# Performance work log

Hardware: AMD Instinct MI355X
Metric: run time of the kernel (lower is better)

## Reference

```python
import jax, jax.numpy as jnp
import numpy as np

HEAD_DIM = 256
NUM_HEADS = 16
NUM_KV_HEADS = 8
EPS = 1e-6
SCALING = 256 ** -0.5  # query_pre_attn_scalar
SOFTCAP = 50.0
NEG_INF = -2.3819763e38


def setup_inputs() -> dict:
    key = jax.random.key(0)
    ks = jax.random.split(key, 8)
    B, S, HID, MAXS = 1, 2048, 3072, 4096
    hidden_states = jax.random.normal(ks[0], (B, S, HID), dtype=jnp.float32)
    # RoPE tables (complex freqs_cis represented as cos/sin), base 10000
    inv_freq = 1.0 / (10000.0 ** (np.arange(0, HEAD_DIM, 2, dtype=np.float32) / HEAD_DIM))
    t = np.arange(S, dtype=np.float32)
    ang = np.outer(t, inv_freq)  # [S, D/2]
    freqs_cos = jnp.asarray(np.cos(ang), dtype=jnp.float32)
    freqs_sin = jnp.asarray(np.sin(ang), dtype=jnp.float32)
    kv_write_indices = jnp.arange(S, dtype=jnp.int32)
    k_cache = jnp.zeros((B, MAXS, NUM_KV_HEADS, HEAD_DIM), dtype=jnp.float32)
    v_cache = jnp.zeros((B, MAXS, NUM_KV_HEADS, HEAD_DIM), dtype=jnp.float32)
    # causal mask over cache slots: query i may attend cache slot j iff j <= i
    i = jnp.arange(S)[:, None]
    j = jnp.arange(MAXS)[None, :]
    mask = jnp.where(j <= i, 0.0, NEG_INF).astype(jnp.float32)[None, None]  # [1,1,S,MAXS]
    sd = 1.0 / np.sqrt(HID)
    wq = jax.random.normal(ks[1], (HID, NUM_HEADS * HEAD_DIM), dtype=jnp.float32) * sd
    wk = jax.random.normal(ks[2], (HID, NUM_KV_HEADS * HEAD_DIM), dtype=jnp.float32) * sd
    wv = jax.random.normal(ks[3], (HID, NUM_KV_HEADS * HEAD_DIM), dtype=jnp.float32) * sd
    wo = jax.random.normal(ks[4], (NUM_HEADS * HEAD_DIM, HID), dtype=jnp.float32) * (1.0 / np.sqrt(NUM_HEADS * HEAD_DIM))
    q_norm_w = jax.random.normal(ks[5], (HEAD_DIM,), dtype=jnp.float32) * 0.02
    k_norm_w = jax.random.normal(ks[6], (HEAD_DIM,), dtype=jnp.float32) * 0.02
    return dict(hidden_states=hidden_states, freqs_cos=freqs_cos, freqs_sin=freqs_sin,
                kv_write_indices=kv_write_indices, k_cache=k_cache, v_cache=v_cache,
                mask=mask, wq=wq, wk=wk, wv=wv, wo=wo, q_norm_w=q_norm_w, k_norm_w=k_norm_w)


def _rmsnorm(x, w):
    xf = x.astype(jnp.float32)
    n = xf * jax.lax.rsqrt(jnp.mean(xf * xf, axis=-1, keepdims=True) + EPS)
    return (n * (1.0 + w.astype(jnp.float32))).astype(x.dtype)


def _rope(x, cos, sin):
    # x: [B,S,H,D]; complex rotation on (first half, second half) pairs
    D2 = x.shape[-1] // 2
    xr, xi = x[..., :D2], x[..., D2:]
    cos = cos[None, :, None, :]
    sin = sin[None, :, None, :]
    return jnp.concatenate([xr * cos - xi * sin, xr * sin + xi * cos], axis=-1).astype(x.dtype)


def reference(hidden_states, freqs_cos, freqs_sin, kv_write_indices, k_cache, v_cache,
              mask, wq, wk, wv, wo, q_norm_w, k_norm_w):
    B, S, _ = hidden_states.shape
    xq = (hidden_states @ wq).reshape(B, S, NUM_HEADS, HEAD_DIM)
    xk = (hidden_states @ wk).reshape(B, S, NUM_KV_HEADS, HEAD_DIM)
    xv = (hidden_states @ wv).reshape(B, S, NUM_KV_HEADS, HEAD_DIM)
    xq = _rmsnorm(xq, q_norm_w)
    xk = _rmsnorm(xk, k_norm_w)
    xq = _rope(xq, freqs_cos, freqs_sin)
    xk = _rope(xk, freqs_cos, freqs_sin)
    # KV-cache write (index_copy_ on dim 1)
    k_cache = k_cache.at[:, kv_write_indices].set(xk)
    v_cache = v_cache.at[:, kv_write_indices].set(xv)
    rep = NUM_HEADS // NUM_KV_HEADS
    key = jnp.repeat(k_cache, rep, axis=2)    # [B,MAXS,H,D]
    value = jnp.repeat(v_cache, rep, axis=2)
    scores = jnp.einsum('bqhd,bkhd->bhqk', xq * SCALING, key)
    scores = jnp.tanh(scores / SOFTCAP) * SOFTCAP
    scores = scores + mask
    probs = jax.nn.softmax(scores.astype(jnp.float32), axis=-1).astype(xq.dtype)
    out = jnp.einsum('bhqk,bkhd->bqhd', probs, value).reshape(B, S, NUM_HEADS * HEAD_DIM)
    return out @ wo
```

## Files before the change

### kernel.cpp

```cpp
#include <hip/hip_runtime.h>
#include <hip/hip_bf16.h>

#define S_LEN 2048
#define HID   3072
#define NH    16
#define NKV   8
#define HD    256
#define EPSV  1e-6f
#define SCALING 0.0625f
#define SOFTCAP 50.0f

typedef __attribute__((ext_vector_type(8))) short bf16x8;
typedef __attribute__((ext_vector_type(4))) float f32x4;

__device__ __forceinline__ unsigned short f2bf(float f) {
  union { float f; unsigned u; } x; x.f = f;
  unsigned r = x.u + 0x7FFFu + ((x.u >> 16) & 1u);
  return (unsigned short)(r >> 16);
}

__device__ __forceinline__ void gload_lds16(const void* g, void* l) {
  __builtin_amdgcn_global_load_lds((const __attribute__((address_space(1))) void*)g,
                                   (__attribute__((address_space(3))) void*)l, 16, 0, 0);
}

__global__ __launch_bounds__(256) void conv_b(const float* __restrict__ in,
                                              unsigned short* __restrict__ out, int n) {
  int i = (blockIdx.x * 256 + threadIdx.x) * 4;
  if (i >= n) return;
  float4 v = *(const float4*)(in + i);
  ushort4 o;
  o.x = f2bf(v.x); o.y = f2bf(v.y); o.z = f2bf(v.z); o.w = f2bf(v.w);
  *(ushort4*)(out + i) = o;
}

__global__ __launch_bounds__(256) void conv_t(const float* __restrict__ W,
                                              unsigned short* __restrict__ WT,
                                              int K, int N) {
  __shared__ float tile[32][33];
  int tx = threadIdx.x & 31, ty = threadIdx.x >> 5;
  int n0 = blockIdx.x * 32, k0 = blockIdx.y * 32;
#pragma unroll
  for (int j = 0; j < 4; j++)
    tile[ty + j * 8][tx] = W[(size_t)(k0 + ty + j * 8) * N + n0 + tx];
  __syncthreads();
#pragma unroll
  for (int j = 0; j < 4; j++)
    WT[(size_t)(n0 + ty + j * 8) * K + k0 + tx] = f2bf(tile[tx][ty + j * 8]);
}

__global__ __launch_bounds__(256) void tr_bf16(const unsigned short* __restrict__ in,
                                               unsigned short* __restrict__ out,
                                               int R, int C) {
  __shared__ unsigned short tile[32][33];
  int tx = threadIdx.x & 31, ty = threadIdx.x >> 5;
  int c0 = blockIdx.x * 32, r0 = blockIdx.y * 32;
#pragma unroll
  for (int j = 0; j < 4; j++)
    tile[ty + j * 8][tx] = in[(size_t)(r0 + ty + j * 8) * C + c0 + tx];
  __syncthreads();
#pragma unroll
  for (int j = 0; j < 4; j++)
    out[(size_t)(c0 + ty + j * 8) * R + r0 + tx] = tile[tx][ty + j * 8];
}

__global__ __launch_bounds__(256) void gemm_qkv(const unsigned short* __restrict__ A,
                                                const unsigned short* __restrict__ B,
                                                float* __restrict__ XQ,
                                                float* __restrict__ XK,
                                                unsigned short* __restrict__ Vb) {
  const int K = HID;
  __shared__ unsigned short As[128 * 32];
  __shared__ unsigned short Bs[128 * 32];
  const int t = threadIdx.x;
  const int w = t >> 6, l = t & 63;
  const int m0 = blockIdx.y * 128, n0 = blockIdx.x * 128;
  const int wr = (w >> 1) * 64, wc = (w & 1) * 64;
  const int lr = l & 15, lk = (l >> 4) * 8;
  f32x4 acc[4][4] = {};

  const int e0 = t * 8;
  const int ar0 = e0 >> 5, ac0 = e0 & 31;
  const size_t abase = (size_t)(m0 + ar0) * K + ac0;
  const size_t bbase = (size_t)(n0 + ar0) * K + ac0;

  for (int k0 = 0; k0 < K; k0 += 32) {
    gload_lds16(A + abase + k0, As + e0);
    gload_lds16(A + abase + (size_t)64 * K + k0, As + e0 + 2048);
    gload_lds16(B + bbase + k0, Bs + e0);
    gload_lds16(B + bbase + (size_t)64 * K + k0, Bs + e0 + 2048);
    __syncthreads();
    bf16x8 af[4], bfv[4];
#pragma unroll
    for (int i = 0; i < 4; i++)
      af[i] = *(const bf16x8*)(As + (wr + i * 16 + lr) * 32 + lk);
#pragma unroll
    for (int i = 0; i < 4; i++)
      bfv[i] = *(const bf16x8*)(Bs + (wc + i * 16 + lr) * 32 + lk);
#pragma unroll
    for (int i = 0; i < 4; i++)
#pragma unroll
      for (int j = 0; j < 4; j++)
        acc[i][j] = __builtin_amdgcn_mfma_f32_16x16x32_bf16(af[i], bfv[j], acc[i][j], 0, 0, 0);
    __syncthreads();
  }

  const int rq = (l >> 4) * 4;
#pragma unroll
  for (int i = 0; i < 4; i++)
#pragma unroll
    for (int j = 0; j < 4; j++) {
      int mrow = m0 + wr + i * 16 + rq;
      int ncol = n0 + wc + j * 16 + lr;
      if (ncol < 4096) {
#pragma unroll
        for (int r = 0; r < 4; r++)
          XQ[(size_t)(mrow + r) * 4096 + ncol] = acc[i][j][r];
      } else if (ncol < 6144) {
#pragma unroll
        for (int r = 0; r < 4; r++)
          XK[(size_t)(mrow + r) * 2048 + ncol - 4096] = acc[i][j][r];
      } else {
#pragma unroll
        for (int r = 0; r < 4; r++)
          Vb[(size_t)(mrow + r) * 2048 + ncol - 6144] = f2bf(acc[i][j][r]);
      }
    }
}

__global__ __launch_bounds__(256) void gemm_nt(const unsigned short* __restrict__ A,
                                               const unsigned short* __restrict__ B,
                                               float* __restrict__ Cf,
                                               int M, int N, int K) {
  __shared__ unsigned short As[128 * 32];
  __shared__ unsigned short Bs[128 * 32];
  const int t = threadIdx.x;
  const int w = t >> 6, l = t & 63;
  const int m0 = blockIdx.y * 128, n0 = blockIdx.x * 128;
  const int wr = (w >> 1) * 64, wc = (w & 1) * 64;
  const int lr = l & 15, lk = (l >> 4) * 8;
  f32x4 acc[4][4] = {};

  const int e0 = t * 8;
  const int ar0 = e0 >> 5, ac0 = e0 & 31;
  const size_t abase = (size_t)(m0 + ar0) * K + ac0;
  const size_t bbase = (size_t)(n0 + ar0) * K + ac0;

  for (int k0 = 0; k0 < K; k0 += 32) {
    gload_lds16(A + abase + k0, As + e0);
    gload_lds16(A + abase + (size_t)64 * K + k0, As + e0 + 2048);
    gload_lds16(B + bbase + k0, Bs + e0);
    gload_lds16(B + bbase + (size_t)64 * K + k0, Bs + e0 + 2048);
    __syncthreads();
    bf16x8 af[4], bfv[4];
#pragma unroll
    for (int i = 0; i < 4; i++)
      af[i] = *(const bf16x8*)(As + (wr + i * 16 + lr) * 32 + lk);
#pragma unroll
    for (int i = 0; i < 4; i++)
      bfv[i] = *(const bf16x8*)(Bs + (wc + i * 16 + lr) * 32 + lk);
#pragma unroll
    for (int i = 0; i < 4; i++)
#pragma unroll
      for (int j = 0; j < 4; j++)
        acc[i][j] = __builtin_amdgcn_mfma_f32_16x16x32_bf16(af[i], bfv[j], acc[i][j], 0, 0, 0);
    __syncthreads();
  }

  const int rq = (l >> 4) * 4;
#pragma unroll
  for (int i = 0; i < 4; i++)
#pragma unroll
    for (int j = 0; j < 4; j++) {
      int mrow = m0 + wr + i * 16 + rq;
      int ncol = n0 + wc + j * 16 + lr;
#pragma unroll
      for (int r = 0; r < 4; r++)
        Cf[(size_t)(mrow + r) * N + ncol] = acc[i][j][r];
    }
}

__global__ __launch_bounds__(256) void norm_rope(const float* __restrict__ x,
                                                 unsigned short* __restrict__ out,
                                                 const float* __restrict__ w,
                                                 const float* __restrict__ fc,
                                                 const float* __restrict__ fs,
                                                 int heads_per_tok, float scale) {
  __shared__ float sh[256];
  __shared__ float red[4];
  int row = blockIdx.x;
  int t = threadIdx.x;
  float v = x[(size_t)row * 256 + t];
  float ss = v * v;
#pragma unroll
  for (int off = 32; off > 0; off >>= 1) ss += __shfl_down(ss, off);
  if ((t & 63) == 0) red[t >> 6] = ss;
  __syncthreads();
  float tot = red[0] + red[1] + red[2] + red[3];
  float rn = rsqrtf(tot * (1.0f / 256.0f) + EPSV);
  sh[t] = v * rn * (1.0f + w[t]);
  __syncthreads();
  if (t < 128) {
    int s = row / heads_per_tok;
    int h = row - s * heads_per_tok;
    size_t ob = ((size_t)h * S_LEN + s) * HD;
    float xr = sh[t], xi = sh[t + 128];
    float c = fc[(size_t)s * 128 + t], sn = fs[(size_t)s * 128 + t];
    out[ob + t]       = f2bf((xr * c - xi * sn) * scale);
    out[ob + t + 128] = f2bf((xr * sn + xi * c) * scale);
  }
}

__global__ __launch_bounds__(256) void attn(const unsigned short* __restrict__ Q,
                                            const unsigned short* __restrict__ Kc,
                                            const unsigned short* __restrict__ VT,
                                            unsigned short* __restrict__ O) {
  __shared__ unsigned short Ks[2][32 * 256];
  __shared__ unsigned short Vs[2][256 * 32];
  __shared__ unsigned short Ps[4][16][40];
  const int t = threadIdx.x, w = t >> 6, l = t & 63;
  const int n = blockIdx.x;
  const int kvh = n & 7;
  const int h = kvh * 2 + ((n >> 3) & 1);
  const int qbase = (31 - (n >> 4)) * 64;
  const int lr = l & 15, g = l >> 4, lk = g * 8;
  const int wq0 = qbase + w * 16;

  const unsigned short* Qh = Q + (size_t)h * S_LEN * HD;
  const char* Khb = (const char*)(Kc + (size_t)kvh * S_LEN * HD);
  const char* Vhb = (const char*)(VT + (size_t)kvh * HD * S_LEN);

  bf16x8 qf[8];
#pragma unroll
  for (int c = 0; c < 8; c++)
    qf[c] = *(const bf16x8*)(Qh + (size_t)(wq0 + lr) * HD + c * 32 + lk);

  f32x4 o_acc[16] = {};
  float m_r[4] = {-1e30f, -1e30f, -1e30f, -1e30f};
  float l_r[4] = {0.f, 0.f, 0.f, 0.f};

  auto stage = [&](int kv0, int b) {
#pragma unroll
    for (int i = 0; i < 4; i++) {
      int L = t * 16 + i * 4096;
      int ks = L ^ (((L >> 9) & 7) << 4);
      gload_lds16(Khb + (size_t)kv0 * 512 + ks, (char*)(Ks[b]) + L);
    }
#pragma unroll
    for (int i = 0; i < 4; i++) {
      int L = t * 16 + i * 4096;
      int d = L >> 6;
      int kb = (L & 63) ^ (((d >> 1) & 3) << 4);
      gload_lds16(Vhb + (size_t)d * (S_LEN * 2) + (size_t)kv0 * 2 + kb, (char*)(Vs[b]) + L);
    }
  };

  const int ntB = (qbase + 64) >> 5;
  stage(0, 0);
  __syncthreads();
  int buf = 0;
  for (int tile = 0; tile < ntB; tile++) {
    const int kv0 = tile << 5;
    if (tile + 1 < ntB) stage(kv0 + 32, buf ^ 1);

    if (kv0 <= wq0 + 15) {
      const bool masked = (kv0 + 31 > wq0);
      const char* Kb = (const char*)(Ks[buf]);
      const char* Vb = (const char*)(Vs[buf]);

      f32x4 sacc[2] = {};
#pragma unroll
      for (int c = 0; c < 8; c++) {
        int a0 = (lr * 512 + c * 64 + g * 16) ^ ((lr & 7) << 4);
        bf16x8 k0f = *(const bf16x8*)(Kb + a0);
        bf16x8 k1f = *(const bf16x8*)(Kb + a0 + 8192);
        sacc[0] = __builtin_amdgcn_mfma_f32_16x16x32_bf16(qf[c], k0f, sacc[0], 0, 0, 0);
        sacc[1] = __builtin_amdgcn_mfma_f32_16x16x32_bf16(qf[c], k1f, sacc[1], 0, 0, 0);
      }

      float p0a[4], p1a[4], corr[4];
#pragma unroll
      for (int r = 0; r < 4; r++) {
        float sv0 = sacc[0][r], sv1 = sacc[1][r];
        {
          float ax = fabsf(sv0) * (2.0f / SOFTCAP);
          float e2 = __expf(-ax);
          sv0 = copysignf((1.f - e2) / (1.f + e2) * SOFTCAP, sv0);
          ax = fabsf(sv1) * (2.0f / SOFTCAP);
          e2 = __expf(-ax);
          sv1 = copysignf((1.f - e2) / (1.f + e2) * SOFTCAP, sv1);
        }
        if (masked) {
          int qi = wq0 + g * 4 + r;
          sv0 = (kv0 + lr <= qi) ? sv0 : -1e30f;
          sv1 = (kv0 + 16 + lr <= qi) ? sv1 : -1e30f;
        }
        float mx = fmaxf(sv0, sv1);
#pragma unroll
        for (int off = 1; off < 16; off <<= 1) mx = fmaxf(mx, __shfl_xor(mx, off));
        float mnew = fmaxf(m_r[r], mx);
        corr[r] = __expf(m_r[r] - mnew);
        float p0 = __expf(sv0 - mnew);
        float p1 = __expf(sv1 - mnew);
        p0a[r] = p0; p1a[r] = p1;
        float rs = p0 + p1;
#pragma unroll
        for (int off = 1; off < 16; off <<= 1) rs += __shfl_xor(rs, off);
        l_r[r] = l_r[r] * corr[r] + rs;
        m_r[r] = mnew;
      }

      bool need = (corr[0] + corr[1] + corr[2] + corr[3]) < 4.0f;
      if (__any(need)) {
        f32x4 c4;
        c4[0] = corr[0]; c4[1] = corr[1]; c4[2] = corr[2]; c4[3] = corr[3];
#pragma unroll
        for (int fn = 0; fn < 16; fn++) o_acc[fn] *= c4;
      }

#pragma unroll
      for (int r = 0; r < 4; r++) {
        int q = g * 4 + r;
        Ps[w][q][lr]      = f2bf(p0a[r]);
        Ps[w][q][16 + lr] = f2bf(p1a[r]);
      }
      bf16x8 pa = *(const bf16x8*)(&Ps[w][lr][lk]);
#pragma unroll
      for (int fn = 0; fn < 16; fn++) {
        int row = fn * 16 + lr;
        int av = (row * 64 + g * 16) ^ (((row >> 1) & 3) << 4);
        bf16x8 vf = *(const bf16x8*)(Vb + av);
        o_acc[fn] = __builtin_amdgcn_mfma_f32_16x16x32_bf16(pa, vf, o_acc[fn], 0, 0, 0);
      }
    }
    __syncthreads();
    buf ^= 1;
  }

  f32x4 inv4;
#pragma unroll
  for (int r = 0; r < 4; r++) inv4[r] = (l_r[r] > 0.f) ? 1.0f / l_r[r] : 0.f;
#pragma unroll
  for (int fn = 0; fn < 16; fn++) {
    f32x4 ov = o_acc[fn] * inv4;
#pragma unroll
    for (int r = 0; r < 4; r++) {
      int q = wq0 + g * 4 + r;
      O[(size_t)q * 4096 + h * HD + fn * 16 + lr] = f2bf(ov[r]);
    }
  }
}

extern "C" void kernel_launch(void* const* d_in, const int* in_sizes, int n_in,
                              void* d_out, int out_size, void* d_ws, size_t ws_size,
                              hipStream_t stream) {
  const float* hidden = (const float*)d_in[0];
  const float* fc  = (const float*)d_in[1];
  const float* fs  = (const float*)d_in[2];
  const float* wq  = (const float*)d_in[7];
  const float* wk  = (const float*)d_in[8];
  const float* wv  = (const float*)d_in[9];
  const float* wo  = (const float*)d_in[10];
  const float* qnw = (const float*)d_in[11];
  const float* knw = (const float*)d_in[12];
  float* out = (float*)d_out;

  char* ws = (char*)d_ws;
  size_t off = 0;
  auto alloc = [&](size_t bytes) {
    char* p = ws + off;
    off += (bytes + 255) & ~(size_t)255;
    return p;
  };
  unsigned short* Xbf    = (unsigned short*)alloc((size_t)S_LEN * HID * 2);
  unsigned short* WqkvT  = (unsigned short*)alloc((size_t)8192 * HID * 2);
  unsigned short* WoT    = (unsigned short*)alloc((size_t)HID * 4096 * 2);
  float*          XQ32   = (float*)alloc((size_t)S_LEN * 4096 * 4);
  float*          XK32   = (float*)alloc((size_t)S_LEN * 2048 * 4);
  unsigned short* Qbf    = (unsigned short*)alloc((size_t)S_LEN * 4096 * 2);
  unsigned short* Kbf    = (unsigned short*)alloc((size_t)S_LEN * 2048 * 2);
  unsigned short* Vbf    = (unsigned short*)alloc((size_t)S_LEN * 2048 * 2);
  unsigned short* Obf = (unsigned short*)XQ32;
  unsigned short* VTb = (unsigned short*)XK32;

  conv_b<<<(S_LEN * HID) / 1024, 256, 0, stream>>>(hidden, Xbf, S_LEN * HID);
  conv_t<<<dim3(4096 / 32, HID / 32), 256, 0, stream>>>(wq, WqkvT, HID, 4096);
  conv_t<<<dim3(2048 / 32, HID / 32), 256, 0, stream>>>(wk, WqkvT + (size_t)4096 * HID, HID, 2048);
  conv_t<<<dim3(2048 / 32, HID / 32), 256, 0, stream>>>(wv, WqkvT + (size_t)6144 * HID, HID, 2048);
  conv_t<<<dim3(HID / 32, 4096 / 32), 256, 0, stream>>>(wo, WoT, 4096, HID);

  gemm_qkv<<<dim3(8192 / 128, S_LEN / 128), 256, 0, stream>>>(Xbf, WqkvT, XQ32, XK32, Vbf);

  norm_rope<<<S_LEN * NH, 256, 0, stream>>>(XQ32, Qbf, qnw, fc, fs, NH, SCALING);
  norm_rope<<<S_LEN * NKV, 256, 0, stream>>>(XK32, Kbf, knw, fc, fs, NKV, 1.0f);

  tr_bf16<<<dim3(2048 / 32, 2048 / 32), 256, 0, stream>>>(Vbf, VTb, S_LEN, 2048);

  attn<<<512, 256, 0, stream>>>(Qbf, Kbf, VTb, Obf);

  gemm_nt<<<dim3(HID / 128, S_LEN / 128), 256, 0, stream>>>(Obf, WoT, out, S_LEN, HID, 4096);
}
```

Before: 726.9 us.

## Vectorize weight transpose, XCD-aware GEMM tile mapping, transposed-S attention softmax

The weight convert-transpose kernel now uses 64x64 tiles with float4 loads and ushort4 stores, cutting the number of memory transactions. Both GEMMs remap block IDs so that the tiles handled by each XCD share N columns, aiming for better L2 reuse of B. The attention kernel computes S transposed (K times Q), so each lane owns a single query row. Row max and sum then need only two cross-lane shuffles instead of sixteen-lane butterflies per row, and P is written to LDS as packed vectors. The cost is extra shuffles to broadcast the correction and normalizer factors, plus a block remapping that assumes gridDim.x is divisible by 8 and gridDim.y is 16.

```diff
diff --git a/kernel.cpp b/kernel.cpp
--- a/kernel.cpp
+++ b/kernel.cpp
@@ -37,16 +37,29 @@
 __global__ __launch_bounds__(256) void conv_t(const float* __restrict__ W,
                                               unsigned short* __restrict__ WT,
                                               int K, int N) {
-  __shared__ float tile[32][33];
-  int tx = threadIdx.x & 31, ty = threadIdx.x >> 5;
-  int n0 = blockIdx.x * 32, k0 = blockIdx.y * 32;
-#pragma unroll
-  for (int j = 0; j < 4; j++)
-    tile[ty + j * 8][tx] = W[(size_t)(k0 + ty + j * 8) * N + n0 + tx];
+  __shared__ float tile[64][65];
+  const int n0 = blockIdx.x * 64, k0 = blockIdx.y * 64;
+  const int tr = threadIdx.x >> 4;
+  const int tc = threadIdx.x & 15;
+#pragma unroll
+  for (int i = 0; i < 4; i++) {
+    float4 v = *(const float4*)(W + (size_t)(k0 + tr + 16 * i) * N + n0 + tc * 4);
+    tile[tr + 16 * i][tc * 4 + 0] = v.x;
+    tile[tr + 16 * i][tc * 4 + 1] = v.y;
+    tile[tr + 16 * i][tc * 4 + 2] = v.z;
+    tile[tr + 16 * i][tc * 4 + 3] = v.w;
+  }
   __syncthreads();
 #pragma unroll
-  for (int j = 0; j < 4; j++)
-    WT[(size_t)(n0 + ty + j * 8) * K + k0 + tx] = f2bf(tile[tx][ty + j * 8]);
+  for (int i = 0; i < 4; i++) {
+    int nrow = tr + 16 * i;
+    ushort4 o;
+    o.x = f2bf(tile[tc * 4 + 0][nrow]);
+    o.y = f2bf(tile[tc * 4 + 1][nrow]);
+    o.z = f2bf(tile[tc * 4 + 2][nrow]);
+    o.w = f2bf(tile[tc * 4 + 3][nrow]);
+    *(ushort4*)(WT + (size_t)(n0 + nrow) * K + k0 + tc * 4) = o;
+  }
 }
 
 __global__ __launch_bounds__(256) void tr_bf16(const unsigned short* __restrict__ in,
@@ -74,7 +87,10 @@
   __shared__ unsigned short Bs[128 * 32];
   const int t = threadIdx.x;
   const int w = t >> 6, l = t & 63;
-  const int m0 = blockIdx.y * 128, n0 = blockIdx.x * 128;
+  const int bid = blockIdx.y * gridDim.x + blockIdx.x;
+  const int xcd = bid & 7, ii = bid >> 3;
+  const int m0 = (ii & 15) * 128;
+  const int n0 = (xcd * (gridDim.x >> 3) + (ii >> 4)) * 128;
   const int wr = (w >> 1) * 64, wc = (w & 1) * 64;
   const int lr = l & 15, lk = (l >> 4) * 8;
   f32x4 acc[4][4] = {};
@@ -136,7 +152,10 @@
   __shared__ unsigned short Bs[128 * 32];
   const int t = threadIdx.x;
   const int w = t >> 6, l = t & 63;
-  const int m0 = blockIdx.y * 128, n0 = blockIdx.x * 128;
+  const int bid = blockIdx.y * gridDim.x + blockIdx.x;
+  const int xcd = bid & 7, ii = bid >> 3;
+  const int m0 = (ii & 15) * 128;
+  const int n0 = (xcd * (gridDim.x >> 3) + (ii >> 4)) * 128;
   const int wr = (w >> 1) * 64, wc = (w & 1) * 64;
   const int lr = l & 15, lk = (l >> 4) * 8;
   f32x4 acc[4][4] = {};
@@ -225,6 +244,7 @@
   const int qbase = (31 - (n >> 4)) * 64;
   const int lr = l & 15, g = l >> 4, lk = g * 8;
   const int wq0 = qbase + w * 16;
+  const int q_own = wq0 + lr;
 
   const unsigned short* Qh = Q + (size_t)h * S_LEN * HD;
   const char* Khb = (const char*)(Kc + (size_t)kvh * S_LEN * HD);
@@ -236,8 +256,7 @@
     qf[c] = *(const bf16x8*)(Qh + (size_t)(wq0 + lr) * HD + c * 32 + lk);
 
   f32x4 o_acc[16] = {};
-  float m_r[4] = {-1e30f, -1e30f, -1e30f, -1e30f};
-  float l_r[4] = {0.f, 0.f, 0.f, 0.f};
+  float m_s = -1e30f, l_s = 0.f;
 
   auto stage = [&](int kv0, int b) {
 #pragma unroll
@@ -274,57 +293,62 @@
         int a0 = (lr * 512 + c * 64 + g * 16) ^ ((lr & 7) << 4);
         bf16x8 k0f = *(const bf16x8*)(Kb + a0);
         bf16x8 k1f = *(const bf16x8*)(Kb + a0 + 8192);
-        sacc[0] = __builtin_amdgcn_mfma_f32_16x16x32_bf16(qf[c], k0f, sacc[0], 0, 0, 0);
-        sacc[1] = __builtin_amdgcn_mfma_f32_16x16x32_bf16(qf[c], k1f, sacc[1], 0, 0, 0);
+        sacc[0] = __builtin_amdgcn_mfma_f32_16x16x32_bf16(k0f, qf[c], sacc[0], 0, 0, 0);
+        sacc[1] = __builtin_amdgcn_mfma_f32_16x16x32_bf16(k1f, qf[c], sacc[1], 0, 0, 0);
       }
 
-      float p0a[4], p1a[4], corr[4];
-#pragma unroll
-      for (int r = 0; r < 4; r++) {
-        float sv0 = sacc[0][r], sv1 = sacc[1][r];
-        {
-          float ax = fabsf(sv0) * (2.0f / SOFTCAP);
+      float sv[8];
+#pragma unroll
+      for (int nb = 0; nb < 2; nb++)
+#pragma unroll
+        for (int r = 0; r < 4; r++) {
+          float s = sacc[nb][r];
+          float ax = fabsf(s) * (2.0f / SOFTCAP);
           float e2 = __expf(-ax);
-          sv0 = copysignf((1.f - e2) / (1.f + e2) * SOFTCAP, sv0);
-          ax = fabsf(sv1) * (2.0f / SOFTCAP);
-          e2 = __expf(-ax);
-          sv1 = copysignf((1.f - e2) / (1.f + e2) * SOFTCAP, sv1);
+          s = copysignf((1.f - e2) / (1.f + e2) * SOFTCAP, s);
+          if (masked) {
+            int kj = kv0 + nb * 16 + 4 * g + r;
+            s = (kj <= q_own) ? s : -1e30f;
+          }
+          sv[nb * 4 + r] = s;
         }
-        if (masked) {
-          int qi = wq0 + g * 4 + r;
-          sv0 = (kv0 + lr <= qi) ? sv0 : -1e30f;
-          sv1 = (kv0 + 16 + lr <= qi) ? sv1 : -1e30f;
-        }
-        float mx = fmaxf(sv0, sv1);
-#pragma unroll
-        for (int off = 1; off < 16; off <<= 1) mx = fmaxf(mx, __shfl_xor(mx, off));
-        float mnew = fmaxf(m_r[r], mx);
-        corr[r] = __expf(m_r[r] - mnew);
-        float p0 = __expf(sv0 - mnew);
-        float p1 = __expf(sv1 - mnew);
-        p0a[r] = p0; p1a[r] = p1;
-        float rs = p0 + p1;
-#pragma unroll
-        for (int off = 1; off < 16; off <<= 1) rs += __shfl_xor(rs, off);
-        l_r[r] = l_r[r] * corr[r] + rs;
-        m_r[r] = mnew;
+
+      float mx = fmaxf(fmaxf(fmaxf(sv[0], sv[1]), fmaxf(sv[2], sv[3])),
+                       fmaxf(fmaxf(sv[4], sv[5]), fmaxf(sv[6], sv[7])));
+      mx = fmaxf(mx, __shfl_xor(mx, 16));
+      mx = fmaxf(mx, __shfl_xor(mx, 32));
+      float mnew = fmaxf(m_s, mx);
+      float corr = __expf(m_s - mnew);
+
+      float ps[8];
+      float rs = 0.f;
+#pragma unroll
+      for (int i = 0; i < 8; i++) {
+        ps[i] = __expf(sv[i] - mnew);
+        rs += ps[i];
       }
-
-      bool need = (corr[0] + corr[1] + corr[2] + corr[3]) < 4.0f;
-      if (__any(need)) {
+      rs += __shfl_xor(rs, 16);
+      rs += __shfl_xor(rs, 32);
+      l_s = l_s * corr + rs;
+      m_s = mnew;
+
+      if (__any(corr < 1.0f)) {
         f32x4 c4;
-        c4[0] = corr[0]; c4[1] = corr[1]; c4[2] = corr[2]; c4[3] = corr[3];
+#pragma unroll
+        for (int r = 0; r < 4; r++) c4[r] = __shfl(corr, 4 * g + r);
 #pragma unroll
         for (int fn = 0; fn < 16; fn++) o_acc[fn] *= c4;
       }
 
-#pragma unroll
-      for (int r = 0; r < 4; r++) {
-        int q = g * 4 + r;
-        Ps[w][q][lr]      = f2bf(p0a[r]);
-        Ps[w][q][16 + lr] = f2bf(p1a[r]);
-      }
-      bf16x8 pa = *(const bf16x8*)(&Ps[w][lr][lk]);
+      uint2 lo, hi;
+      lo.x = (unsigned)f2bf(ps[0]) | ((unsigned)f2bf(ps[1]) << 16);
+      lo.y = (unsigned)f2bf(ps[2]) | ((unsigned)f2bf(ps[3]) << 16);
+      hi.x = (unsigned)f2bf(ps[4]) | ((unsigned)f2bf(ps[5]) << 16);
+      hi.y = (unsigned)f2bf(ps[6]) | ((unsigned)f2bf(ps[7]) << 16);
+      *(uint2*)(&Ps[w][lr][4 * g])      = lo;
+      *(uint2*)(&Ps[w][lr][16 + 4 * g]) = hi;
+
+      bf16x8 pa = *(const bf16x8*)(&Ps[w][lr][8 * g]);
 #pragma unroll
       for (int fn = 0; fn < 16; fn++) {
         int row = fn * 16 + lr;
@@ -337,9 +361,10 @@
     buf ^= 1;
   }
 
+  float inv = (l_s > 0.f) ? 1.0f / l_s : 0.f;
   f32x4 inv4;
 #pragma unroll
-  for (int r = 0; r < 4; r++) inv4[r] = (l_r[r] > 0.f) ? 1.0f / l_r[r] : 0.f;
+  for (int r = 0; r < 4; r++) inv4[r] = __shfl(inv, 4 * g + r);
 #pragma unroll
   for (int fn = 0; fn < 16; fn++) {
     f32x4 ov = o_acc[fn] * inv4;
@@ -384,10 +409,10 @@
   unsigned short* VTb = (unsigned short*)XK32;
 
   conv_b<<<(S_LEN * HID) / 1024, 256, 0, stream>>>(hidden, Xbf, S_LEN * HID);
-  conv_t<<<dim3(4096 / 32, HID / 32), 256, 0, stream>>>(wq, WqkvT, HID, 4096);
-  conv_t<<<dim3(2048 / 32, HID / 32), 256, 0, stream>>>(wk, WqkvT + (size_t)4096 * HID, HID, 2048);
-  conv_t<<<dim3(2048 / 32, HID / 32), 256, 0, stream>>>(wv, WqkvT + (size_t)6144 * HID, HID, 2048);
-  conv_t<<<dim3(HID / 32, 4096 / 32), 256, 0, stream>>>(wo, WoT, 4096, HID);
+  conv_t<<<dim3(4096 / 64, HID / 64), 256, 0, stream>>>(wq, WqkvT, HID, 4096);
+  conv_t<<<dim3(2048 / 64, HID / 64), 256, 0, stream>>>(wk, WqkvT + (size_t)4096 * HID, HID, 2048);
+  conv_t<<<dim3(2048 / 64, HID / 64), 256, 0, stream>>>(wv, WqkvT + (size_t)6144 * HID, HID, 2048);
+  conv_t<<<dim3(HID / 64, 4096 / 64), 256, 0, stream>>>(wo, WoT, 4096, HID);
 
   gemm_qkv<<<dim3(8192 / 128, S_LEN / 128), 256, 0, stream>>>(Xbf, WqkvT, XQ32, XK32, Vbf);
 
```

After: 681.2 us. -6.3%, faster.
